# Optimization experiments

Measured on AMD Instinct MI355X. Metric: run time of the kernel, lower is better.

## Reference

```python
import jax, jax.numpy as jnp
import numpy as np

SCALE = 32.0      # backbone feature->image coordinate scale (stride)
LOG_EPS = 1e-8    # geometry.safe_log epsilon


def _safe_log(x):
    return jnp.log(jnp.maximum(x, LOG_EPS))


def setup_inputs() -> dict:
    key = jax.random.key(0)
    k1, k2, k3, k4, k5, k6 = jax.random.split(key, 6)
    B, P, L = 128, 4096, 128
    cls_scores = jax.random.normal(k1, (B, 2 * P), dtype=jnp.float32)
    bbox_deltas = jax.random.normal(k2, (B, 4 * P), dtype=jnp.float32) * 0.1
    # RoI in feature coordinates: x,y in [0,40), w,h in [1,11)
    roi_xy = jax.random.uniform(k3, (B, P, 2), dtype=jnp.float32) * 40.0
    roi_wh = jax.random.uniform(k4, (B, P, 2), dtype=jnp.float32) * 10.0 + 1.0
    roi = jnp.concatenate([roi_xy, roi_wh], axis=-1)
    # Ground-truth labels in image coordinates: x,y in [0,1280), w,h in [32,352)
    lab_xy = jax.random.uniform(k5, (B, L, 2), dtype=jnp.float32) * 1280.0
    lab_wh = jax.random.uniform(k6, (B, L, 2), dtype=jnp.float32) * 320.0 + 32.0
    labels = jnp.concatenate([lab_xy, lab_wh], axis=-1)
    return {
        "cls_scores": cls_scores,
        "bbox_deltas": bbox_deltas,
        "roi": roi,
        "labels": labels,
        "neg_enabled": 1,
    }


def reference(cls_scores, bbox_deltas, roi, labels, neg_enabled):
    """Vectorized port of ClassifierModel._compute_loss summed over the batch.

    cls_scores  [B, 2P] laid out [class, proposal] (cls[i::P] -> per-proposal logits)
    bbox_deltas [B, 4P] laid out [coord, proposal]
    roi         [B, P, 4] proposals in feature coords (x,y,w,h)
    labels      [B, L, 4] ground-truth boxes in image coords (x,y,w,h)
    """
    B, P = roi.shape[0], roi.shape[1]
    roi_img = roi.astype(jnp.float32) * SCALE  # feature -> image coords

    # --- IoU matrix [B, L, P] (geometry.calculate_IoU over all label/proposal pairs)
    l = labels[:, :, None, :]   # [B, L, 1, 4]
    r = roi_img[:, None, :, :]  # [B, 1, P, 4]
    ix = jnp.maximum(0.0, jnp.minimum(l[..., 0] + l[..., 2], r[..., 0] + r[..., 2]) - jnp.maximum(l[..., 0], r[..., 0]))
    iy = jnp.maximum(0.0, jnp.minimum(l[..., 1] + l[..., 3], r[..., 1] + r[..., 3]) - jnp.maximum(l[..., 1], r[..., 1]))
    inter = ix * iy
    union = l[..., 2] * l[..., 3] + r[..., 2] * r[..., 3] - inter
    iou = jnp.where(union > 0.0, inter / union, 0.0)  # [B, L, P]

    # --- matching: argmax over labels where any IoU is nonzero, else -1
    any_hit = jnp.sum((iou != 0.0).astype(jnp.int32), axis=1) > 0        # [B, P]
    match = jnp.where(any_hit, jnp.argmax(iou, axis=1), -1)              # [B, P]
    pos = match > 0  # NOTE: original uses match[i] > 0 (strict), kept faithfully

    matched = jnp.take_along_axis(labels, jnp.clip(match, 0)[:, :, None], axis=1)  # [B, P, 4]
    tx = (matched[..., 0] - roi_img[..., 0]) / roi_img[..., 2]
    ty = (matched[..., 1] - roi_img[..., 1]) / roi_img[..., 3]
    tw = _safe_log(matched[..., 2] / roi_img[..., 2])
    th = _safe_log(matched[..., 3] / roi_img[..., 3])
    targets = jnp.stack([tx, ty, tw, th], axis=-1)                        # [B, P, 4]
    preds = bbox_deltas.reshape(B, 4, P).transpose(0, 2, 1)               # [B, P, 4]

    # Huber (delta=1, mean over the 4 coords) per proposal
    err = targets - preds
    ae = jnp.abs(err)
    huber = jnp.mean(jnp.where(ae <= 1.0, 0.5 * err * err, ae - 0.5), axis=-1)  # [B, P]

    # --- classification: softmax over the two per-proposal logits, then
    # CategoricalCrossentropy(probs, const) = -sum(probs * log(const))
    logits = cls_scores.reshape(B, 2, P).transpose(0, 2, 1)               # [B, P, 2]
    probs = jax.nn.softmax(logits, axis=-1)
    log_pos = jnp.log(jnp.array([0.1, 0.9], dtype=jnp.float32))
    log_neg = jnp.log(jnp.array([0.9, 0.1], dtype=jnp.float32))
    ce_pos = -jnp.sum(probs * log_pos, axis=-1)                           # [B, P]
    ce_neg = -jnp.sum(probs * log_neg, axis=-1)                           # [B, P]

    neg_term = jnp.where(jnp.asarray(neg_enabled) > 0, ce_neg, 0.0)
    per_prop = jnp.where(pos, 2.0 * huber + ce_pos, neg_term)             # [B, P]
    return jnp.sum(per_prop)
```

## Files before the change

### kernel.cpp

```cpp
#include <hip/hip_runtime.h>
#include <hip/hip_bf16.h>
#include <math.h>

#define BB 128
#define PP 4096
#define LL 128
#define BLOCK 256
#define CHUNKS (PP / BLOCK)
#define SCALE 32.0f
#define LCHUNK 8

__global__ __launch_bounds__(256) void prep_labels_kernel(
    const float* __restrict__ labels, float* __restrict__ labp)
{
    int i = blockIdx.x * 256 + threadIdx.x;
    if (i < BB * LL) {
        const float* lp = labels + (size_t)i * 4;
        float x = lp[0], y = lp[1], w = lp[2], h = lp[3];
        float* o = labp + (size_t)i * 8;
        o[0] = x;
        o[1] = y;
        o[2] = x + w;
        o[3] = y + h;
        o[4] = w * h;
        o[5] = w;
        o[6] = h;
        o[7] = 0.0f;
    }
}

__global__ __launch_bounds__(BLOCK) void classifier_loss_kernel(
    const float* __restrict__ cls,
    const float* __restrict__ bbox,
    const float* __restrict__ roi,
    const float* __restrict__ labp,
    const int* __restrict__ neg_enabled,
    float* __restrict__ out)
{
    __shared__ float s_red[BLOCK / 64];

    const int b     = blockIdx.x >> 4;
    const int chunk = blockIdx.x & (CHUNKS - 1);
    const int p     = chunk * BLOCK + threadIdx.x;

    const float* __restrict__ lb = labp + (size_t)b * LL * 8;

    const float* rp = roi + ((size_t)b * PP + p) * 4;
    const float rx = rp[0] * SCALE, ry = rp[1] * SCALE;
    const float rw = rp[2] * SCALE, rh = rp[3] * SCALE;
    const float rx2 = rx + rw, ry2 = ry + rh;
    const float rarea = rw * rh;

    float best_inter = -1.0f, best_denom = 1.0f;
    int   best_idx = 0;

    for (int lc = 0; lc < LL; lc += LCHUNK) {
        #pragma unroll
        for (int u = 0; u < LCHUNK; ++u) {
            const int li = lc + u;
            const float s_x    = lb[li * 8 + 0];
            const float s_y    = lb[li * 8 + 1];
            const float s_x2   = lb[li * 8 + 2];
            const float s_y2   = lb[li * 8 + 3];
            const float s_area = lb[li * 8 + 4];
            float ix = fmaxf(0.0f, fminf(s_x2, rx2) - fmaxf(s_x, rx));
            float iy = fmaxf(0.0f, fminf(s_y2, ry2) - fmaxf(s_y, ry));
            float inter = ix * iy;
            float denom = s_area + rarea;
            bool gt = inter * best_denom > best_inter * denom;
            best_inter = gt ? inter : best_inter;
            best_denom = gt ? denom : best_denom;
            best_idx   = gt ? li    : best_idx;
        }
    }

    const bool pos = (best_inter > 0.0f) && (best_idx > 0);

    const float s0 = cls[(size_t)b * 2 * PP + p];
    const float s1 = cls[(size_t)b * 2 * PP + PP + p];
    const float mx = fmaxf(s0, s1);
    const float e0 = expf(s0 - mx);
    const float e1 = expf(s1 - mx);
    const float inv = 1.0f / (e0 + e1);
    const float p0 = e0 * inv, p1 = e1 * inv;
    const float LOG01 = -2.3025850929940457f;
    const float LOG09 = -0.10536051565782628f;
    const float ce_pos = -(p0 * LOG01 + p1 * LOG09);
    const float ce_neg = -(p0 * LOG09 + p1 * LOG01);

    float per;
    if (pos) {
        const float* mp = lb + best_idx * 8;
        float mxl = mp[0], myl = mp[1], mwl = mp[5], mhl = mp[6];
        float tx = (mxl - rx) / rw;
        float ty = (myl - ry) / rh;
        float tw = logf(fmaxf(mwl / rw, 1e-8f));
        float th = logf(fmaxf(mhl / rh, 1e-8f));
        const float* bp = bbox + (size_t)b * 4 * PP + p;
        float ex = tx - bp[0];
        float ey = ty - bp[PP];
        float ew = tw - bp[2 * PP];
        float eh = th - bp[3 * PP];
        float ax = fabsf(ex), ay = fabsf(ey), aw = fabsf(ew), ah = fabsf(eh);
        float hx = (ax <= 1.0f) ? 0.5f * ex * ex : ax - 0.5f;
        float hy = (ay <= 1.0f) ? 0.5f * ey * ey : ay - 0.5f;
        float hw = (aw <= 1.0f) ? 0.5f * ew * ew : aw - 0.5f;
        float hh = (ah <= 1.0f) ? 0.5f * eh * eh : ah - 0.5f;
        float huber = 0.25f * (hx + hy + hw + hh);
        per = 2.0f * huber + ce_pos;
    } else {
        per = (neg_enabled[0] > 0) ? ce_neg : 0.0f;
    }

    float v = per;
    #pragma unroll
    for (int off = 32; off > 0; off >>= 1)
        v += __shfl_down(v, off, 64);
    if ((threadIdx.x & 63) == 0)
        s_red[threadIdx.x >> 6] = v;
    __syncthreads();
    if (threadIdx.x == 0) {
        float blk = s_red[0] + s_red[1] + s_red[2] + s_red[3];
        atomicAdd(out, blk);
    }
}

extern "C" void kernel_launch(void* const* d_in, const int* in_sizes, int n_in,
                              void* d_out, int out_size, void* d_ws, size_t ws_size,
                              hipStream_t stream) {
    const float* cls    = (const float*)d_in[0];
    const float* bbox   = (const float*)d_in[1];
    const float* roi    = (const float*)d_in[2];
    const float* labels = (const float*)d_in[3];
    const int*   neg    = (const int*)d_in[4];
    float* out  = (float*)d_out;
    float* labp = (float*)d_ws;

    hipMemsetAsync(out, 0, sizeof(float) * out_size, stream);
    prep_labels_kernel<<<dim3((BB * LL + 255) / 256), dim3(256), 0, stream>>>(
        labels, labp);
    classifier_loss_kernel<<<dim3(BB * CHUNKS), dim3(BLOCK), 0, stream>>>(
        cls, bbox, roi, labp, neg, out);
}
```

Baseline: 116.7 us.

## Store prepped labels as SoA, fully unroll IoU loop, hoist loads

Result: faster. 110.3 us (-5.5%).

```diff
diff --git a/kernel.cpp b/kernel.cpp
--- a/kernel.cpp
+++ b/kernel.cpp
@@ -8,24 +8,21 @@
 #define BLOCK 256
 #define CHUNKS (PP / BLOCK)
 #define SCALE 32.0f
-#define LCHUNK 8
 
 __global__ __launch_bounds__(256) void prep_labels_kernel(
     const float* __restrict__ labels, float* __restrict__ labp)
 {
     int i = blockIdx.x * 256 + threadIdx.x;
     if (i < BB * LL) {
+        int b = i >> 7, li = i & (LL - 1);
         const float* lp = labels + (size_t)i * 4;
         float x = lp[0], y = lp[1], w = lp[2], h = lp[3];
-        float* o = labp + (size_t)i * 8;
-        o[0] = x;
-        o[1] = y;
-        o[2] = x + w;
-        o[3] = y + h;
-        o[4] = w * h;
-        o[5] = w;
-        o[6] = h;
-        o[7] = 0.0f;
+        float* o = labp + (size_t)b * (5 * LL) + li;
+        o[0 * LL] = x;
+        o[1 * LL] = y;
+        o[2 * LL] = x + w;
+        o[3 * LL] = y + h;
+        o[4 * LL] = w * h;
     }
 }
 
@@ -34,6 +31,7 @@
     const float* __restrict__ bbox,
     const float* __restrict__ roi,
     const float* __restrict__ labp,
+    const float* __restrict__ labels,
     const int* __restrict__ neg_enabled,
     float* __restrict__ out)
 {
@@ -43,41 +41,40 @@
     const int chunk = blockIdx.x & (CHUNKS - 1);
     const int p     = chunk * BLOCK + threadIdx.x;
 
-    const float* __restrict__ lb = labp + (size_t)b * LL * 8;
+    const float* __restrict__ lb = labp + (size_t)b * (5 * LL);
 
     const float* rp = roi + ((size_t)b * PP + p) * 4;
-    const float rx = rp[0] * SCALE, ry = rp[1] * SCALE;
-    const float rw = rp[2] * SCALE, rh = rp[3] * SCALE;
+    const float r0 = rp[0], r1 = rp[1], r2 = rp[2], r3 = rp[3];
+    const float s0 = cls[(size_t)b * 2 * PP + p];
+    const float s1 = cls[(size_t)b * 2 * PP + PP + p];
+
+    const float rx = r0 * SCALE, ry = r1 * SCALE;
+    const float rw = r2 * SCALE, rh = r3 * SCALE;
     const float rx2 = rx + rw, ry2 = ry + rh;
     const float rarea = rw * rh;
 
     float best_inter = -1.0f, best_denom = 1.0f;
     int   best_idx = 0;
 
-    for (int lc = 0; lc < LL; lc += LCHUNK) {
-        #pragma unroll
-        for (int u = 0; u < LCHUNK; ++u) {
-            const int li = lc + u;
-            const float s_x    = lb[li * 8 + 0];
-            const float s_y    = lb[li * 8 + 1];
-            const float s_x2   = lb[li * 8 + 2];
-            const float s_y2   = lb[li * 8 + 3];
-            const float s_area = lb[li * 8 + 4];
-            float ix = fmaxf(0.0f, fminf(s_x2, rx2) - fmaxf(s_x, rx));
-            float iy = fmaxf(0.0f, fminf(s_y2, ry2) - fmaxf(s_y, ry));
-            float inter = ix * iy;
-            float denom = s_area + rarea;
-            bool gt = inter * best_denom > best_inter * denom;
-            best_inter = gt ? inter : best_inter;
-            best_denom = gt ? denom : best_denom;
-            best_idx   = gt ? li    : best_idx;
-        }
+    #pragma unroll
+    for (int li = 0; li < LL; ++li) {
+        const float s_x    = lb[0 * LL + li];
+        const float s_y    = lb[1 * LL + li];
+        const float s_x2   = lb[2 * LL + li];
+        const float s_y2   = lb[3 * LL + li];
+        const float s_area = lb[4 * LL + li];
+        float ix = fmaxf(0.0f, fminf(s_x2, rx2) - fmaxf(s_x, rx));
+        float iy = fmaxf(0.0f, fminf(s_y2, ry2) - fmaxf(s_y, ry));
+        float inter = ix * iy;
+        float denom = s_area + rarea;
+        bool gt = inter * best_denom > best_inter * denom;
+        best_inter = gt ? inter : best_inter;
+        best_denom = gt ? denom : best_denom;
+        best_idx   = gt ? li    : best_idx;
     }
 
     const bool pos = (best_inter > 0.0f) && (best_idx > 0);
 
-    const float s0 = cls[(size_t)b * 2 * PP + p];
-    const float s1 = cls[(size_t)b * 2 * PP + PP + p];
     const float mx = fmaxf(s0, s1);
     const float e0 = expf(s0 - mx);
     const float e1 = expf(s1 - mx);
@@ -90,8 +87,8 @@
 
     float per;
     if (pos) {
-        const float* mp = lb + best_idx * 8;
-        float mxl = mp[0], myl = mp[1], mwl = mp[5], mhl = mp[6];
+        const float* mp = labels + ((size_t)b * LL + best_idx) * 4;
+        float mxl = mp[0], myl = mp[1], mwl = mp[2], mhl = mp[3];
         float tx = (mxl - rx) / rw;
         float ty = (myl - ry) / rh;
         float tw = logf(fmaxf(mwl / rw, 1e-8f));
@@ -140,5 +137,5 @@
     prep_labels_kernel<<<dim3((BB * LL + 255) / 256), dim3(256), 0, stream>>>(
         labels, labp);
     classifier_loss_kernel<<<dim3(BB * CHUNKS), dim3(BLOCK), 0, stream>>>(
-        cls, bbox, roi, labp, neg, out);
+        cls, bbox, roi, labp, labels, neg, out);
 }
```
